# Kernel tuning notes

Hardware: AMD Instinct MI355X
Metric: run time of the kernel (lower is better)

The kernel has to match this reference:

```python
import jax, jax.numpy as jnp
import numpy as np
from jax import lax

NPOINTS = [1024, 256, 64, 16]
RADII = [0.02, 0.04, 0.06, 0.08]
NSAMPLE = [32, 32, 16, 16]
# per-level MLP widths; first entry already includes the +3 for use_xyz concat
MLPS = [[6, 32, 32, 64], [67, 64, 64, 128], [131, 128, 128, 256], [259, 256, 256, 512]]
EPS = 1e-5


def setup_inputs() -> dict:
    key = jax.random.key(0)
    B, N = 8, 16384
    pc = jax.random.uniform(jax.random.fold_in(key, 0), (B, N, 6), jnp.float32)
    # xyz into a 0.2-cube so the hard-coded radii (0.02..0.08) find real neighborhoods
    pc = pc.at[..., :3].multiply(0.2)
    inp = {"pointcloud": pc}
    ki = 1
    for l, m in enumerate(MLPS):
        for j in range(len(m) - 1):
            cin, cout = m[j], m[j + 1]
            inp[f"w{l}{j}"] = jax.random.normal(jax.random.fold_in(key, ki), (cin, cout), jnp.float32) * (1.0 / float(np.sqrt(cin)))
            inp[f"g{l}{j}"] = jnp.ones((cout,), jnp.float32)
            inp[f"b{l}{j}"] = jnp.zeros((cout,), jnp.float32)
            ki += 1
    return inp


def _fps(xyz, npoint):
    # iterative farthest point sampling, start at index 0 (matches CUDA kernel)
    B, N, _ = xyz.shape

    def step(carry, _):
        mind, last = carry
        lastp = jnp.take_along_axis(xyz, last[:, None, None], axis=1)  # [B,1,3]
        d = jnp.sum((xyz - lastp) ** 2, axis=-1)                       # [B,N]
        mind = jnp.minimum(mind, d)
        nxt = jnp.argmax(mind, axis=1).astype(jnp.int32)
        return (mind, nxt), last

    init = (jnp.full((B, N), 1e10, xyz.dtype), jnp.zeros((B,), jnp.int32))
    _, idx = lax.scan(step, init, None, length=npoint)
    return jnp.transpose(idx)  # [B,npoint]


def _gather(pts, idx):
    # pts [B,N,C], idx [B,...] -> [B,...,C]
    return jax.vmap(lambda p, i: p[i])(pts, idx)


def _ball_query(xyz, centers, radius, nsample):
    # first nsample points (in index order) within radius; pad with first hit (0 if none)
    N = xyz.shape[1]
    d2 = jnp.sum((centers[:, :, None, :] - xyz[:, None, :, :]) ** 2, axis=-1)  # [B,S,N]
    key = jnp.where(d2 < radius * radius, jnp.arange(N, dtype=jnp.int32), N)
    negtop, _ = lax.top_k(-key, nsample)
    sel = -negtop                      # ascending candidate indices
    valid = sel < N
    first = jnp.where(valid[..., :1], sel[..., :1], 0)
    return jnp.where(valid, sel, first)  # [B,S,nsample] int32


def _sa(xyz, feats, npoint, radius, nsample, layers):
    fps_idx = lax.stop_gradient(_fps(xyz, npoint))
    new_xyz = _gather(xyz, fps_idx)                    # [B,S,3]
    idx = _ball_query(xyz, new_xyz, radius, nsample)   # [B,S,K]
    g = _gather(xyz, idx) - new_xyz[:, :, None, :]     # centered grouped xyz [B,S,K,3]
    g = jnp.concatenate([g, _gather(feats, idx)], axis=-1)  # use_xyz concat -> [B,S,K,3+C]
    x = g
    for W, gamma, beta in layers:
        x = jnp.einsum('bski,io->bsko', x, W)          # 1x1 conv, bias=False (bn on)
        mu = jnp.mean(x, axis=(0, 1, 2))               # BN training-mode batch stats
        var = jnp.var(x, axis=(0, 1, 2))
        x = jax.nn.relu(gamma * (x - mu) * lax.rsqrt(var + EPS) + beta)
    return new_xyz, jnp.max(x, axis=2)                 # max-pool over neighbors -> [B,S,Cout]


def reference(pointcloud, w00, g00, b00, w01, g01, b01, w02, g02, b02,
              w10, g10, b10, w11, g11, b11, w12, g12, b12,
              w20, g20, b20, w21, g21, b21, w22, g22, b22,
              w30, g30, b30, w31, g31, b31, w32, g32, b32):
    params = [
        [(w00, g00, b00), (w01, g01, b01), (w02, g02, b02)],
        [(w10, g10, b10), (w11, g11, b11), (w12, g12, b12)],
        [(w20, g20, b20), (w21, g21, b21), (w22, g22, b22)],
        [(w30, g30, b30), (w31, g31, b31), (w32, g32, b32)],
    ]
    xyz = pointcloud[..., :3]
    feats = pointcloud[..., 3:]   # channels-last (torch keeps [B,C,N]; pure layout diff)
    l_xyz, l_feats = [xyz], [feats]
    for k in range(4):
        nx, nf = _sa(l_xyz[k], l_feats[k], NPOINTS[k], RADII[k], NSAMPLE[k], params[k])
        l_xyz.append(nx)
        l_feats.append(nf)
    return tuple(l_xyz) + tuple(l_feats)
```

## Files before the change

kernel.cpp:

```cpp
#include <hip/hip_runtime.h>

#define WAVE 64

__global__ __launch_bounds__(256) void split_kernel(const float* __restrict__ pc,
    float* __restrict__ xyz, float* __restrict__ feats, int total) {
  int t = blockIdx.x * blockDim.x + threadIdx.x;
  if (t >= total) return;
  const float* p = pc + (size_t)t * 6;
  xyz[t * 3 + 0] = p[0]; xyz[t * 3 + 1] = p[1]; xyz[t * 3 + 2] = p[2];
  feats[t * 3 + 0] = p[3]; feats[t * 3 + 1] = p[4]; feats[t * 3 + 2] = p[5];
}

__global__ __launch_bounds__(256) void zero_kernel(float* __restrict__ p, int n) {
  int t = blockIdx.x * blockDim.x + threadIdx.x;
  if (t < n) p[t] = 0.f;
}

__device__ __forceinline__ float dpp_max_f32(float v) {
#define DPP_STEP_F(ctrl) { int t_ = __builtin_amdgcn_update_dpp( \
      __float_as_int(v), __float_as_int(v), ctrl, 0xf, 0xf, false); \
    v = fmaxf(v, __int_as_float(t_)); }
  DPP_STEP_F(0x111) DPP_STEP_F(0x112) DPP_STEP_F(0x114)
  DPP_STEP_F(0x118) DPP_STEP_F(0x142) DPP_STEP_F(0x143)
#undef DPP_STEP_F
  return v;
}
__device__ __forceinline__ unsigned dpp_max_u32(unsigned v) {
#define DPP_STEP_U(ctrl) { unsigned t_ = (unsigned)__builtin_amdgcn_update_dpp( \
      (int)v, (int)v, ctrl, 0xf, 0xf, false); \
    v = (t_ > v) ? t_ : v; }
  DPP_STEP_U(0x111) DPP_STEP_U(0x112) DPP_STEP_U(0x114)
  DPP_STEP_U(0x118) DPP_STEP_U(0x142) DPP_STEP_U(0x143)
#undef DPP_STEP_U
  return v;
}
__device__ __forceinline__ unsigned bcast63(unsigned v) {
  return (unsigned)__builtin_amdgcn_readlane((int)v, 63);
}

__global__ __launch_bounds__(1024, 4) void fps_big_kernel(const float* __restrict__ xyz,
    float* __restrict__ new_xyz, int N, int S) {
  const int b = blockIdx.x;
  const int tid = threadIdx.x;
  const int lane = tid & 63;
  const float* px = xyz + (size_t)b * N * 3;
  __shared__ unsigned long long s_key[3];
  float rx[16], ry[16], rz[16], mind[16];
#pragma unroll
  for (int p = 0; p < 16; ++p) {
    int i = tid + p * 1024;
    rx[p] = px[i * 3 + 0]; ry[p] = px[i * 3 + 1]; rz[p] = px[i * 3 + 2];
    asm volatile("" : "+v"(rx[p]), "+v"(ry[p]), "+v"(rz[p]));
    mind[p] = 1e10f;
  }
  if (tid < 3) s_key[tid] = 0ull;
  float qx = px[0], qy = px[1], qz = px[2];
  if (tid == 0) {
    float* o = new_xyz + (size_t)b * S * 3;
    o[0] = qx; o[1] = qy; o[2] = qz;
  }
  __syncthreads();
  for (unsigned it = 1; it < (unsigned)S; ++it) {
    float bestv = -1.f; unsigned besti = 0;
#pragma unroll
    for (int p = 0; p < 16; ++p) {
      float dx = __fsub_rn(rx[p], qx);
      float dy = __fsub_rn(ry[p], qy);
      float dz = __fsub_rn(rz[p], qz);
      float d = __fadd_rn(__fadd_rn(__fmul_rn(dx, dx), __fmul_rn(dy, dy)), __fmul_rn(dz, dz));
      float mo = fminf(mind[p], d);
      mind[p] = mo;
      if (mo > bestv) { bestv = mo; besti = (unsigned)(tid + p * 1024); }
    }
    float wm = dpp_max_f32(bestv);
    unsigned wmb = bcast63(__float_as_uint(wm));
    unsigned cand = (__float_as_uint(bestv) == wmb) ? (0xFFFFFFFFu - besti) : 0u;
    unsigned winv = bcast63(dpp_max_u32(cand));
    if (lane == 0) atomicMax(&s_key[it % 3u], ((unsigned long long)wmb << 32) | winv);
    if (tid == 0) s_key[(it + 1) % 3u] = 0ull;
    __syncthreads();
    unsigned long long k = s_key[it % 3u];
    int last = (int)(0xFFFFFFFFu - (unsigned)k);
    const float* q = px + (size_t)last * 3;
    qx = q[0]; qy = q[1]; qz = q[2];
    if (tid == 0) {
      float* o = new_xyz + ((size_t)b * S + it) * 3;
      o[0] = qx; o[1] = qy; o[2] = qz;
    }
  }
}

__global__ void fps_small_kernel(const float* __restrict__ xyz,
    float* __restrict__ new_xyz, int N, int S) {
  const int b = blockIdx.x;
  const int tid = threadIdx.x;
  const int lane = tid & 63;
  const float* px = xyz + (size_t)b * N * 3;
  __shared__ float sx[1024], sy[1024], sz[1024];
  __shared__ unsigned long long s_key[3];
  float x = px[tid * 3 + 0], y = px[tid * 3 + 1], z = px[tid * 3 + 2];
  sx[tid] = x; sy[tid] = y; sz[tid] = z;
  if (tid < 3) s_key[tid] = 0ull;
  float mind = 1e10f;
  float qx = px[0], qy = px[1], qz = px[2];
  if (tid == 0) {
    float* o = new_xyz + (size_t)b * S * 3;
    o[0] = qx; o[1] = qy; o[2] = qz;
  }
  __syncthreads();
  for (unsigned it = 1; it < (unsigned)S; ++it) {
    float dx = __fsub_rn(x, qx);
    float dy = __fsub_rn(y, qy);
    float dz = __fsub_rn(z, qz);
    float d = __fadd_rn(__fadd_rn(__fmul_rn(dx, dx), __fmul_rn(dy, dy)), __fmul_rn(dz, dz));
    mind = fminf(mind, d);
    float wm = dpp_max_f32(mind);
    unsigned wmb = bcast63(__float_as_uint(wm));
    unsigned cand = (__float_as_uint(mind) == wmb) ? (0xFFFFFFFFu - (unsigned)tid) : 0u;
    unsigned winv = bcast63(dpp_max_u32(cand));
    if (lane == 0) atomicMax(&s_key[it % 3u], ((unsigned long long)wmb << 32) | winv);
    if (tid == 0) s_key[(it + 1) % 3u] = 0ull;
    __syncthreads();
    unsigned long long k = s_key[it % 3u];
    int last = (int)(0xFFFFFFFFu - (unsigned)k);
    qx = sx[last]; qy = sy[last]; qz = sz[last];
    if (tid == 0) {
      float* o = new_xyz + ((size_t)b * S + it) * 3;
      o[0] = qx; o[1] = qy; o[2] = qz;
    }
  }
}

__global__ __launch_bounds__(256) void ballquery_kernel(const float* __restrict__ xyz,
    const float* __restrict__ centers, int* __restrict__ out_idx,
    int N, int S, int nsample, float r2) {
  int gw = (blockIdx.x * blockDim.x + threadIdx.x) >> 6;
  int lane = threadIdx.x & 63;
  int b = gw / S;
  int s = gw - b * S;
  const float* px = xyz + (size_t)b * N * 3;
  const float* cp = centers + ((size_t)b * S + s) * 3;
  float cx = cp[0], cy = cp[1], cz = cp[2];
  int* out = out_idx + ((size_t)b * S + s) * nsample;
  int cnt = 0;
  int firsti = 0;
  for (int base = 0; base < N; base += WAVE) {
    int i = base + lane;
    float dx = __fsub_rn(cx, px[i * 3 + 0]);
    float dy = __fsub_rn(cy, px[i * 3 + 1]);
    float dz = __fsub_rn(cz, px[i * 3 + 2]);
    float d = __fadd_rn(__fadd_rn(__fmul_rn(dx, dx), __fmul_rn(dy, dy)), __fmul_rn(dz, dz));
    bool hit = d < r2;
    unsigned long long m = __ballot(hit);
    if (hit) {
      int slot = cnt + __popcll(m & ((1ull << lane) - 1ull));
      if (slot < nsample) out[slot] = i;
    }
    if (cnt == 0 && m) firsti = base + __ffsll((unsigned long long)m) - 1;
    cnt += __popcll(m);
    if (cnt >= nsample) break;
  }
  for (int q = cnt + lane; q < nsample; q += WAVE) out[q] = firsti;
}

__global__ __launch_bounds__(256) void group_kernel(const float* __restrict__ xyz,
    const float* __restrict__ feats, const float* __restrict__ centers,
    const int* __restrict__ idx, float* __restrict__ X,
    int N, int S, int K, int ci, int R) {
  int t = blockIdx.x * blockDim.x + threadIdx.x;
  int C0 = ci + 3;
  int r = t / C0;
  if (r >= R) return;
  int c = t - r * C0;
  int g = r / K;
  int b = g / S;
  int j = idx[r];
  float v;
  if (c < 3) v = __fsub_rn(xyz[((size_t)b * N + j) * 3 + c], centers[(size_t)g * 3 + c]);
  else       v = feats[((size_t)b * N + j) * ci + (c - 3)];
  X[(size_t)r * C0 + c] = v;
}

#define BM 64
#define BN 64
#define BK 16
__global__ __launch_bounds__(256) void mm_fused_kernel(const float* __restrict__ A,
    const float* __restrict__ W, float* __restrict__ Y,
    float* __restrict__ st_out, const float* __restrict__ st_in,
    const float* __restrict__ g_in, const float* __restrict__ b_in,
    int R, int C, int Co, float inv_n) {
  __shared__ float As[BK][BM + 4];
  __shared__ float Bs[BK][BN + 4];
  __shared__ float s_mu[260], s_rs[260], s_g[260], s_b[260];
  __shared__ float s_sum[BN], s_sq[BN];
  int r0 = blockIdx.x * BM;
  int n0 = blockIdx.y * BN;
  int tid = threadIdx.x;
  int tx = tid & 15, ty = tid >> 4;
  if (st_in) {
    for (int c = tid; c < C; c += 256) {
      float mu = st_in[c] * inv_n;
      float var = st_in[512 + c] * inv_n - mu * mu;
      s_mu[c] = mu; s_rs[c] = rsqrtf(var + 1e-5f);
      s_g[c] = g_in[c]; s_b[c] = b_in[c];
    }
  }
  if (tid < BN) { s_sum[tid] = 0.f; s_sq[tid] = 0.f; }
  __syncthreads();
  float acc[4][4] = {};
  for (int k0 = 0; k0 < C; k0 += BK) {
#pragma unroll
    for (int u = 0; u < 4; ++u) {
      int lin = tid + u * 256;
      int row = lin >> 4;
      int cc = lin & 15;
      int c = k0 + cc;
      float v = 0.f;
      if (c < C) {
        v = A[(size_t)(r0 + row) * C + c];
        if (st_in) {
          v = s_g[c] * ((v - s_mu[c]) * s_rs[c]) + s_b[c];
          v = v > 0.f ? v : 0.f;
        }
      }
      As[cc][row] = v;
    }
#pragma unroll
    for (int u = 0; u < 4; ++u) {
      int lin = tid + u * 256;
      int kk = lin >> 6;
      int n = lin & 63;
      int c = k0 + kk;
      Bs[kk][n] = (c < C && (n0 + n) < Co) ? W[(size_t)c * Co + n0 + n] : 0.f;
    }
    __syncthreads();
#pragma unroll
    for (int kk = 0; kk < BK; ++kk) {
      float a0[4], b0[4];
#pragma unroll
      for (int i = 0; i < 4; ++i) a0[i] = As[kk][ty * 4 + i];
#pragma unroll
      for (int jj = 0; jj < 4; ++jj) b0[jj] = Bs[kk][tx * 4 + jj];
#pragma unroll
      for (int i = 0; i < 4; ++i)
#pragma unroll
        for (int jj = 0; jj < 4; ++jj)
          acc[i][jj] = fmaf(a0[i], b0[jj], acc[i][jj]);
    }
    __syncthreads();
  }
#pragma unroll
  for (int i = 0; i < 4; ++i) {
    int r = r0 + ty * 4 + i;
#pragma unroll
    for (int jj = 0; jj < 4; ++jj) {
      int n = n0 + tx * 4 + jj;
      if (n < Co) Y[(size_t)r * Co + n] = acc[i][jj];
    }
  }
#pragma unroll
  for (int jj = 0; jj < 4; ++jj) {
    float cs = 0.f, cq = 0.f;
#pragma unroll
    for (int i = 0; i < 4; ++i) { float v = acc[i][jj]; cs += v; cq += v * v; }
    atomicAdd(&s_sum[tx * 4 + jj], cs);
    atomicAdd(&s_sq[tx * 4 + jj], cq);
  }
  __syncthreads();
  if (tid < BN) {
    int n = n0 + tid;
    if (n < Co) {
      atomicAdd(&st_out[n], s_sum[tid]);
      atomicAdd(&st_out[512 + n], s_sq[tid]);
    }
  }
}

__global__ __launch_bounds__(256) void norm_relu_max_kernel(const float* __restrict__ Y,
    float* __restrict__ O, const float* __restrict__ st,
    const float* __restrict__ gamma, const float* __restrict__ beta,
    int G, int K, int Co, float inv_n) {
  int t = blockIdx.x * blockDim.x + threadIdx.x;
  if (t >= G * Co) return;
  int c = t & (Co - 1);
  int g = t / Co;
  float mu = st[c] * inv_n;
  float var = st[512 + c] * inv_n - mu * mu;
  float rs = rsqrtf(var + 1e-5f);
  float ga = gamma[c], be = beta[c];
  const float* yp = Y + (size_t)g * K * Co + c;
  float m = -1e30f;
  for (int k = 0; k < K; ++k) {
    float v = ga * ((yp[(size_t)k * Co] - mu) * rs) + be;
    m = fmaxf(m, v);
  }
  O[t] = m > 0.f ? m : 0.f;
}

extern "C" void kernel_launch(void* const* d_in, const int* in_sizes, int n_in,
                              void* d_out, int out_size, void* d_ws, size_t ws_size,
                              hipStream_t stream) {
  const float* pc = (const float*)d_in[0];
  float* out = (float*)d_out;
  char* wsb = (char*)d_ws;

  int* ballidx = (int*)wsb;
  float* stats = (float*)(wsb + ((size_t)1 << 20));
  float* bufA = (float*)(wsb + ((size_t)3 << 20));
  float* bufB = (float*)(wsb + ((size_t)37 << 20));

  const int B = 8;
  static const int Ns[4] = {16384, 1024, 256, 64};
  static const int Ss[4] = {1024, 256, 64, 16};
  static const int Ks[4] = {32, 32, 16, 16};
  static const double Rr[4] = {0.02, 0.04, 0.06, 0.08};
  static const int Ci[4] = {3, 64, 128, 256};
  static const int mlp[4][4] = {{6,32,32,64},{67,64,64,128},{131,128,128,256},{259,256,256,512}};
  static const size_t ox[5] = {0, 393216, 417792, 423936, 425472};
  static const size_t of[5] = {425856, 819072, 1343360, 1605504, 1736576};

  split_kernel<<<(B * 16384 + 255) / 256, 256, 0, stream>>>(pc, out + ox[0], out + of[0], B * 16384);
  zero_kernel<<<(12 * 1024 + 255) / 256, 256, 0, stream>>>(stats, 12 * 1024);

  for (int l = 0; l < 4; ++l) {
    const float* xyz = out + ox[l];
    const float* fts = out + of[l];
    float* nxyz = out + ox[l + 1];
    const int N = Ns[l], S = Ss[l], K = Ks[l], ci = Ci[l], C0 = ci + 3;
    const float r2 = (float)(Rr[l] * Rr[l]);

    if (l == 0) fps_big_kernel<<<B, 1024, 0, stream>>>(xyz, nxyz, N, S);
    else        fps_small_kernel<<<B, N, 0, stream>>>(xyz, nxyz, N, S);

    ballquery_kernel<<<(B * S) / 4, 256, 0, stream>>>(xyz, nxyz, ballidx, N, S, K, r2);

    const int R = B * S * K;
    {
      int total = R * C0;
      group_kernel<<<(total + 255) / 256, 256, 0, stream>>>(xyz, fts, nxyz, ballidx, bufA,
                                                            N, S, K, ci, R);
    }

    const float inv_n = 1.0f / (float)R;
    float* X = bufA; float* Y = bufB;
    const float* prev_st = nullptr;
    const float* prev_g = nullptr;
    const float* prev_b = nullptr;
    for (int j = 0; j < 3; ++j) {
      const int cin = mlp[l][j], cout = mlp[l][j + 1];
      const float* Wt = (const float*)d_in[1 + (l * 3 + j) * 3 + 0];
      const float* Ga = (const float*)d_in[1 + (l * 3 + j) * 3 + 1];
      const float* Be = (const float*)d_in[1 + (l * 3 + j) * 3 + 2];
      float* st = stats + (size_t)(l * 3 + j) * 1024;
      dim3 grid(R / 64, (cout + 63) / 64);
      mm_fused_kernel<<<grid, 256, 0, stream>>>(X, Wt, Y, st, prev_st, prev_g, prev_b,
                                                R, cin, cout, inv_n);
      if (j < 2) {
        prev_st = st; prev_g = Ga; prev_b = Be;
        float* tswap = X; X = Y; Y = tswap;
      } else {
        int G = B * S;
        int tot = G * cout;
        norm_relu_max_kernel<<<(tot + 255) / 256, 256, 0, stream>>>(Y, out + of[l + 1], st, Ga, Be,
                                                                    G, K, cout, inv_n);
      }
    }
  }
}
```

Before: 2.796 ms.

## Halve FPS block size and use packed FP32 math for distance updates

The level-0 farthest point sampling kernel now runs 512 threads per block, and each thread holds 32 points as float2 pairs. Distance computation uses v_pk_add_f32 and v_pk_mul_f32 packed instructions, so two points are processed per instruction. This reduces the number of waves taking part in each iteration's barrier and atomic reduction, and cuts VALU instruction count. The cost is more register pressure and serial per-thread work, and the rounding order must stay identical so the argmax ties still match.

```diff
diff --git a/kernel.cpp b/kernel.cpp
--- a/kernel.cpp
+++ b/kernel.cpp
@@ -14,6 +14,13 @@
 __global__ __launch_bounds__(256) void zero_kernel(float* __restrict__ p, int n) {
   int t = blockIdx.x * blockDim.x + threadIdx.x;
   if (t < n) p[t] = 0.f;
+}
+
+__device__ __forceinline__ float2 pk_add(float2 a, float2 b) {
+  float2 r; asm("v_pk_add_f32 %0, %1, %2" : "=v"(r) : "v"(a), "v"(b)); return r;
+}
+__device__ __forceinline__ float2 pk_mul(float2 a, float2 b) {
+  float2 r; asm("v_pk_mul_f32 %0, %1, %2" : "=v"(r) : "v"(a), "v"(b)); return r;
 }
 
 __device__ __forceinline__ float dpp_max_f32(float v) {
@@ -38,21 +45,26 @@
   return (unsigned)__builtin_amdgcn_readlane((int)v, 63);
 }
 
-__global__ __launch_bounds__(1024, 4) void fps_big_kernel(const float* __restrict__ xyz,
+__global__ __launch_bounds__(512, 2) void fps_big_kernel(const float* __restrict__ xyz,
     float* __restrict__ new_xyz, int N, int S) {
   const int b = blockIdx.x;
   const int tid = threadIdx.x;
   const int lane = tid & 63;
+  const int wv = tid >> 6;
   const float* px = xyz + (size_t)b * N * 3;
   __shared__ unsigned long long s_key[3];
-  float rx[16], ry[16], rz[16], mind[16];
+  float2 rx[16], ry[16], rz[16], mind[16];
 #pragma unroll
   for (int p = 0; p < 16; ++p) {
-    int i = tid + p * 1024;
-    rx[p] = px[i * 3 + 0]; ry[p] = px[i * 3 + 1]; rz[p] = px[i * 3 + 2];
+    int i0 = tid + (2 * p) * 512;
+    int i1 = tid + (2 * p + 1) * 512;
+    rx[p] = make_float2(px[i0 * 3 + 0], px[i1 * 3 + 0]);
+    ry[p] = make_float2(px[i0 * 3 + 1], px[i1 * 3 + 1]);
+    rz[p] = make_float2(px[i0 * 3 + 2], px[i1 * 3 + 2]);
     asm volatile("" : "+v"(rx[p]), "+v"(ry[p]), "+v"(rz[p]));
-    mind[p] = 1e10f;
-  }
+    mind[p] = make_float2(1e10f, 1e10f);
+  }
+  (void)wv;
   if (tid < 3) s_key[tid] = 0ull;
   float qx = px[0], qy = px[1], qz = px[2];
   if (tid == 0) {
@@ -61,16 +73,25 @@
   }
   __syncthreads();
   for (unsigned it = 1; it < (unsigned)S; ++it) {
+    float2 nqx = make_float2(-qx, -qx);
+    float2 nqy = make_float2(-qy, -qy);
+    float2 nqz = make_float2(-qz, -qz);
     float bestv = -1.f; unsigned besti = 0;
 #pragma unroll
     for (int p = 0; p < 16; ++p) {
-      float dx = __fsub_rn(rx[p], qx);
-      float dy = __fsub_rn(ry[p], qy);
-      float dz = __fsub_rn(rz[p], qz);
-      float d = __fadd_rn(__fadd_rn(__fmul_rn(dx, dx), __fmul_rn(dy, dy)), __fmul_rn(dz, dz));
-      float mo = fminf(mind[p], d);
-      mind[p] = mo;
-      if (mo > bestv) { bestv = mo; besti = (unsigned)(tid + p * 1024); }
+      float2 dx = pk_add(rx[p], nqx);
+      float2 dy = pk_add(ry[p], nqy);
+      float2 dz = pk_add(rz[p], nqz);
+      float2 xx = pk_mul(dx, dx);
+      float2 yy = pk_mul(dy, dy);
+      float2 s1 = pk_add(xx, yy);
+      float2 zz = pk_mul(dz, dz);
+      float2 d  = pk_add(s1, zz);
+      float m0 = fminf(mind[p].x, d.x);
+      float m1 = fminf(mind[p].y, d.y);
+      mind[p].x = m0; mind[p].y = m1;
+      if (m0 > bestv) { bestv = m0; besti = (unsigned)(tid + (2 * p) * 512); }
+      if (m1 > bestv) { bestv = m1; besti = (unsigned)(tid + (2 * p + 1) * 512); }
     }
     float wm = dpp_max_f32(bestv);
     unsigned wmb = bcast63(__float_as_uint(wm));
@@ -329,7 +350,7 @@
     const int N = Ns[l], S = Ss[l], K = Ks[l], ci = Ci[l], C0 = ci + 3;
     const float r2 = (float)(Rr[l] * Rr[l]);
 
-    if (l == 0) fps_big_kernel<<<B, 1024, 0, stream>>>(xyz, nxyz, N, S);
+    if (l == 0) fps_big_kernel<<<B, 512, 0, stream>>>(xyz, nxyz, N, S);
     else        fps_small_kernel<<<B, N, 0, stream>>>(xyz, nxyz, N, S);
 
     ballquery_kernel<<<(B * S) / 4, 256, 0, stream>>>(xyz, nxyz, ballidx, N, S, K, r2);
```

Measured after the change: 2.845 ms. Within noise of the previous version (+1.8%).

## Split level-0 FPS across four workgroups per batch with global atomic barrier

Applied to the files above, without the earlier changes.

The level-0 farthest point sampling kernel now runs four 1024-thread workgroups per batch instead of one, each holding a quarter of the points in registers. After each iteration's block-level argmax, the workgroups combine their keys through a global atomicMax and wait on a global arrival counter, so all four agree on the next point. This spreads the serial FPS loop over more compute units to cut per-iteration ALU work, in exchange for a device-scope spin barrier on every one of the 1023 iterations. It depends on all 32 workgroups being co-resident, and it extends the zero kernel to clear the sync words.

```diff
diff --git a/kernel.cpp b/kernel.cpp
--- a/kernel.cpp
+++ b/kernel.cpp
@@ -1,6 +1,7 @@
 #include <hip/hip_runtime.h>
 
 #define WAVE 64
+#define FPS_SPLIT 4
 
 __global__ __launch_bounds__(256) void split_kernel(const float* __restrict__ pc,
     float* __restrict__ xyz, float* __restrict__ feats, int total) {
@@ -39,23 +40,29 @@
 }
 
 __global__ __launch_bounds__(1024, 4) void fps_big_kernel(const float* __restrict__ xyz,
-    float* __restrict__ new_xyz, int N, int S) {
-  const int b = blockIdx.x;
+    float* __restrict__ new_xyz, unsigned long long* __restrict__ gsync, int N, int S) {
+  const int blk = blockIdx.x;
+  const int b = blk >> 2;
+  const int sub = blk & 3;
   const int tid = threadIdx.x;
   const int lane = tid & 63;
   const float* px = xyz + (size_t)b * N * 3;
+  unsigned long long* gkey = gsync + (size_t)b * 4;
+  unsigned long long* garr = gkey + 3;
   __shared__ unsigned long long s_key[3];
-  float rx[16], ry[16], rz[16], mind[16];
-#pragma unroll
-  for (int p = 0; p < 16; ++p) {
-    int i = tid + p * 1024;
+  __shared__ unsigned long long s_bkey;
+  const int base = sub << 12;
+  float rx[4], ry[4], rz[4], mind[4];
+#pragma unroll
+  for (int p = 0; p < 4; ++p) {
+    int i = base + tid + (p << 10);
     rx[p] = px[i * 3 + 0]; ry[p] = px[i * 3 + 1]; rz[p] = px[i * 3 + 2];
     asm volatile("" : "+v"(rx[p]), "+v"(ry[p]), "+v"(rz[p]));
     mind[p] = 1e10f;
   }
   if (tid < 3) s_key[tid] = 0ull;
   float qx = px[0], qy = px[1], qz = px[2];
-  if (tid == 0) {
+  if (sub == 0 && tid == 0) {
     float* o = new_xyz + (size_t)b * S * 3;
     o[0] = qx; o[1] = qy; o[2] = qz;
   }
@@ -63,14 +70,14 @@
   for (unsigned it = 1; it < (unsigned)S; ++it) {
     float bestv = -1.f; unsigned besti = 0;
 #pragma unroll
-    for (int p = 0; p < 16; ++p) {
+    for (int p = 0; p < 4; ++p) {
       float dx = __fsub_rn(rx[p], qx);
       float dy = __fsub_rn(ry[p], qy);
       float dz = __fsub_rn(rz[p], qz);
       float d = __fadd_rn(__fadd_rn(__fmul_rn(dx, dx), __fmul_rn(dy, dy)), __fmul_rn(dz, dz));
       float mo = fminf(mind[p], d);
       mind[p] = mo;
-      if (mo > bestv) { bestv = mo; besti = (unsigned)(tid + p * 1024); }
+      if (mo > bestv) { bestv = mo; besti = (unsigned)(base + tid + (p << 10)); }
     }
     float wm = dpp_max_f32(bestv);
     unsigned wmb = bcast63(__float_as_uint(wm));
@@ -79,11 +86,24 @@
     if (lane == 0) atomicMax(&s_key[it % 3u], ((unsigned long long)wmb << 32) | winv);
     if (tid == 0) s_key[(it + 1) % 3u] = 0ull;
     __syncthreads();
-    unsigned long long k = s_key[it % 3u];
+    if (tid == 0) {
+      atomicMax(&gkey[it % 3u], s_key[it % 3u]);
+      __threadfence();
+      atomicAdd(garr, 1ull);
+      const unsigned long long tgt = (unsigned long long)FPS_SPLIT * it;
+      while (__hip_atomic_load(garr, __ATOMIC_ACQUIRE, __HIP_MEMORY_SCOPE_AGENT) < tgt) {
+        __builtin_amdgcn_s_sleep(1);
+      }
+      s_bkey = atomicMax(&gkey[it % 3u], 0ull);
+      __hip_atomic_store(&gkey[(it + 2) % 3u], 0ull,
+                         __ATOMIC_RELAXED, __HIP_MEMORY_SCOPE_AGENT);
+    }
+    __syncthreads();
+    unsigned long long k = s_bkey;
     int last = (int)(0xFFFFFFFFu - (unsigned)k);
     const float* q = px + (size_t)last * 3;
     qx = q[0]; qy = q[1]; qz = q[2];
-    if (tid == 0) {
+    if (sub == 0 && tid == 0) {
       float* o = new_xyz + ((size_t)b * S + it) * 3;
       o[0] = qx; o[1] = qy; o[2] = qz;
     }
@@ -306,6 +326,7 @@
 
   int* ballidx = (int*)wsb;
   float* stats = (float*)(wsb + ((size_t)1 << 20));
+  unsigned long long* fps_sync = (unsigned long long*)(stats + 12 * 1024);
   float* bufA = (float*)(wsb + ((size_t)3 << 20));
   float* bufB = (float*)(wsb + ((size_t)37 << 20));
 
@@ -320,7 +341,7 @@
   static const size_t of[5] = {425856, 819072, 1343360, 1605504, 1736576};
 
   split_kernel<<<(B * 16384 + 255) / 256, 256, 0, stream>>>(pc, out + ox[0], out + of[0], B * 16384);
-  zero_kernel<<<(12 * 1024 + 255) / 256, 256, 0, stream>>>(stats, 12 * 1024);
+  zero_kernel<<<(12 * 1024 + 64 + 255) / 256, 256, 0, stream>>>(stats, 12 * 1024 + 64);
 
   for (int l = 0; l < 4; ++l) {
     const float* xyz = out + ox[l];
@@ -329,7 +350,7 @@
     const int N = Ns[l], S = Ss[l], K = Ks[l], ci = Ci[l], C0 = ci + 3;
     const float r2 = (float)(Rr[l] * Rr[l]);
 
-    if (l == 0) fps_big_kernel<<<B, 1024, 0, stream>>>(xyz, nxyz, N, S);
+    if (l == 0) fps_big_kernel<<<B * FPS_SPLIT, 1024, 0, stream>>>(xyz, nxyz, fps_sync, N, S);
     else        fps_small_kernel<<<B, N, 0, stream>>>(xyz, nxyz, N, S);
 
     ballquery_kernel<<<(B * S) / 4, 256, 0, stream>>>(xyz, nxyz, ballidx, N, S, K, r2);
```

Measured after the change: 4.687 ms. 1.68x slower.
